# Optimization experiments

Hardware: AMD Instinct MI355X
Metric: run time of the kernel (lower is better)

Reference implementation:

```python
import jax, jax.numpy as jnp
import numpy as np

B, S, D, H = 2, 2048, 1024, 16
DH = D // H
EPS = 1e-5


def layer_norm(x, g, b):
    # OpenAI-style LN: epsilon inside the sqrt
    u = jnp.mean(x, axis=-1, keepdims=True)
    s = jnp.mean((x - u) ** 2, axis=-1, keepdims=True)
    return g * ((x - u) / jnp.sqrt(s + EPS)) + b


def setup_inputs() -> dict:
    key = jax.random.key(0)
    ks = jax.random.split(key, 8)
    std = 0.002  # Conv1D init std
    return {
        "x": jax.random.normal(ks[0], (B, S, D), dtype=jnp.float32),
        "mask": jnp.ones((B, S), dtype=jnp.bool_),
        "Wqkv": jax.random.normal(ks[1], (D, 3 * D), dtype=jnp.float32) * std,
        "bqkv": jnp.zeros((3 * D,), dtype=jnp.float32),
        "Wvw": jax.random.normal(ks[2], (D, D), dtype=jnp.float32) * std,
        "bvw": jnp.zeros((D,), dtype=jnp.float32),
        "g1": jnp.ones((D,), dtype=jnp.float32),
        "b1": jnp.zeros((D,), dtype=jnp.float32),
        "WA": jax.random.normal(ks[3], (D, 4 * D), dtype=jnp.float32) * std,
        "bA": jnp.zeros((4 * D,), dtype=jnp.float32),
        "WB": jax.random.normal(ks[4], (4 * D, D), dtype=jnp.float32) * std,
        "bB": jnp.zeros((D,), dtype=jnp.float32),
        "g2": jnp.ones((D,), dtype=jnp.float32),
        "b2": jnp.zeros((D,), dtype=jnp.float32),
    }


def reference(x, mask, Wqkv, bqkv, Wvw, bvw, g1, b1, WA, bA, WB, bB, g2, b2):
    maskf = mask.astype(x.dtype)                       # [B,S]
    x = x * maskf[:, :, None]
    # --- multi-head attention ---
    qkv = (x @ Wqkv + bqkv).reshape(B, S, 3, H, DH)    # [B,S,3,H,DH]
    q, k, v = qkv[:, :, 0], qkv[:, :, 1], qkv[:, :, 2]
    w = jnp.einsum('bshd,bzhd->bhsz', q, k) / jnp.sqrt(jnp.asarray(DH, x.dtype))
    causal = jnp.tril(jnp.ones((S, S), dtype=x.dtype)) # [S,S]
    wholemask = maskf[:, None, None, :] * causal[None, None]  # [B,1,S,S]
    w = w + jnp.log(wholemask)                         # additive log-mask (-inf where masked)
    w = jax.nn.softmax(w, axis=-1)
    vw = jnp.einsum('bhsz,bzhd->bshd', w, v).reshape(B, S, D)
    a = vw @ Wvw + bvw
    # --- residual + LN + MLP + LN ---
    n = layer_norm(x + a, g1, b1)
    m = jax.nn.relu(n @ WA + bA) @ WB + bB
    h = layer_norm(n + m, g2, b2)
    return h
```

## Files before the change

### kernel.cpp

```cpp
#include <hip/hip_runtime.h>
#include <stdint.h>

typedef unsigned short u16;
typedef __attribute__((ext_vector_type(8))) short short8;
typedef __attribute__((ext_vector_type(4))) float f32x4;

#define NB 2
#define NS 2048
#define ND 1024
#define NH 16
#define NDH 64
#define NBS (NB*NS)

__device__ __forceinline__ float bf2f(u16 u) {
  union { uint32_t i; float f; } c; c.i = ((uint32_t)u) << 16; return c.f;
}
__device__ __forceinline__ u16 f2bf(float f) {
  union { float f; uint32_t i; } c; c.f = f;
  uint32_t r = (c.i + 0x7fffu + ((c.i >> 16) & 1u)) >> 16;
  return (u16)r;
}

__global__ __launch_bounds__(256)
void k_f32_to_bf16(const float* __restrict__ X, u16* __restrict__ Y, int n4) {
  int i = blockIdx.x * 256 + threadIdx.x;
  if (i >= n4) return;
  float4 v = ((const float4*)X)[i];
  uint2 o;
  o.x = (uint32_t)f2bf(v.x) | ((uint32_t)f2bf(v.y) << 16);
  o.y = (uint32_t)f2bf(v.z) | ((uint32_t)f2bf(v.w) << 16);
  ((uint2*)Y)[i] = o;
}

__global__ __launch_bounds__(256)
void k_transpose_all(const float* __restrict__ Wqkv, const float* __restrict__ Wvw,
                     const float* __restrict__ WA, const float* __restrict__ WB,
                     u16* __restrict__ WqkvT, u16* __restrict__ WvwT,
                     u16* __restrict__ WAT, u16* __restrict__ WBT) {
  __shared__ float tile[32][33];
  int id = blockIdx.x;
  const float* W; u16* WT; int K, N, tid;
  if (id < 3072)      { W = Wqkv; WT = WqkvT; K = 1024; N = 3072; tid = id; }
  else if (id < 4096) { W = Wvw;  WT = WvwT;  K = 1024; N = 1024; tid = id - 3072; }
  else if (id < 8192) { W = WA;   WT = WAT;   K = 1024; N = 4096; tid = id - 4096; }
  else                { W = WB;   WT = WBT;   K = 4096; N = 1024; tid = id - 8192; }
  const int ntx = N >> 5;
  const int n0 = (tid % ntx) << 5, k0 = (tid / ntx) << 5;
  const int tx = threadIdx.x & 31, ty = threadIdx.x >> 5;
  #pragma unroll
  for (int j = 0; j < 4; ++j)
    tile[ty + 8*j][tx] = W[(size_t)(k0 + ty + 8*j) * N + (n0 + tx)];
  __syncthreads();
  #pragma unroll
  for (int j = 0; j < 4; ++j)
    WT[(size_t)(n0 + ty + 8*j) * K + (k0 + tx)] = f2bf(tile[tx][ty + 8*j]);
}

__global__ __launch_bounds__(256)
void k_vt(const u16* __restrict__ qkv, u16* __restrict__ Vt) {
  __shared__ u16 tile[64][72];
  const int zb = blockIdx.x;
  const int bh = blockIdx.y;
  const int b = bh >> 4, h = bh & 15;
  const int t = threadIdx.x;
  const int r = t >> 2, seg = (t & 3) * 16;
  const u16* src = qkv + ((size_t)(b * NS + zb * 64 + r)) * 3072 + 2048 + h * 64 + seg;
  *(short8*)(&tile[r][seg])     = *(const short8*)(src);
  *(short8*)(&tile[r][seg + 8]) = *(const short8*)(src + 8);
  __syncthreads();
  const int dh = t >> 2, zs = (t & 3) * 16;
  short8 o0, o1;
  #pragma unroll
  for (int i = 0; i < 8; ++i) o0[i] = (short)tile[zs + i][dh];
  #pragma unroll
  for (int i = 0; i < 8; ++i) o1[i] = (short)tile[zs + 8 + i][dh];
  u16* dst = Vt + (size_t)(bh * 64 + dh) * NS + zb * 64 + zs;
  *(short8*)(dst)     = o0;
  *(short8*)(dst + 8) = o1;
}

__device__ __forceinline__ void gload_lds16(const void* g, void* l) {
  __builtin_amdgcn_global_load_lds(
      (const __attribute__((address_space(1))) void*)(void*)(uintptr_t)g,
      (__attribute__((address_space(3))) void*)l, 16, 0, 0);
}

template<bool OUT_BF16, bool RELU>
__global__ __launch_bounds__(256)
void k_gemm_bt(const u16* __restrict__ A, const u16* __restrict__ BT,
               const float* __restrict__ bias, void* __restrict__ C,
               int M, int N, int Kstride, int Klen, size_t zCstride)
{
  __shared__ u16 As[128 * 64];
  __shared__ u16 Bs[128 * 64];
  const int t = threadIdx.x, wave = t >> 6, lane = t & 63;
  const int m0 = blockIdx.y * 128, n0 = blockIdx.x * 128;
  const int wr = wave >> 1, wc = wave & 1;
  const int koff = blockIdx.z * Klen;
  A  += koff;
  BT += koff;

  f32x4 acc[4][4] = {};

  int srow[4], scol[4];
  #pragma unroll
  for (int p = 0; p < 4; ++p) {
    int o = p * 4096 + wave * 1024 + lane * 16;
    int r = o >> 7;
    int cb = o & 127;
    srow[p] = r;
    scol[p] = (cb ^ ((r & 7) << 4)) >> 1;
  }

  const int nkt = Klen >> 6;
  for (int kt = 0; kt < nkt; ++kt) {
    const int k0 = kt << 6;
    #pragma unroll
    for (int p = 0; p < 4; ++p) {
      const u16* srcA = A  + (size_t)(m0 + srow[p]) * Kstride + k0 + scol[p];
      const u16* srcB = BT + (size_t)(n0 + srow[p]) * Kstride + k0 + scol[p];
      gload_lds16(srcA, (char*)As + p * 4096 + wave * 1024);
      gload_lds16(srcB, (char*)Bs + p * 4096 + wave * 1024);
    }
    asm volatile("s_waitcnt vmcnt(0)" ::: "memory");
    __syncthreads();

    #pragma unroll
    for (int kk = 0; kk < 2; ++kk) {
      const int cbase = kk * 64 + ((lane >> 4) << 4);
      short8 af[4], bf[4];
      #pragma unroll
      for (int mi = 0; mi < 4; ++mi) {
        int r = wr * 64 + mi * 16 + (lane & 15);
        af[mi] = *(const short8*)((const char*)As + r * 128 + (cbase ^ ((r & 7) << 4)));
      }
      #pragma unroll
      for (int nj = 0; nj < 4; ++nj) {
        int r = wc * 64 + nj * 16 + (lane & 15);
        bf[nj] = *(const short8*)((const char*)Bs + r * 128 + (cbase ^ ((r & 7) << 4)));
      }
      #pragma unroll
      for (int mi = 0; mi < 4; ++mi)
        #pragma unroll
        for (int nj = 0; nj < 4; ++nj)
          acc[mi][nj] = __builtin_amdgcn_mfma_f32_16x16x32_bf16(af[mi], bf[nj], acc[mi][nj], 0, 0, 0);
    }
    __syncthreads();
  }

  const int lr = (lane >> 4) << 2;
  const int lc = lane & 15;
  #pragma unroll
  for (int nj = 0; nj < 4; ++nj) {
    const int col = n0 + wc * 64 + nj * 16 + lc;
    const float bs = bias ? bias[col] : 0.f;
    #pragma unroll
    for (int mi = 0; mi < 4; ++mi) {
      const int row = m0 + wr * 64 + mi * 16 + lr;
      #pragma unroll
      for (int i = 0; i < 4; ++i) {
        float v = acc[mi][nj][i] + bs;
        if (RELU) v = fmaxf(v, 0.f);
        if (OUT_BF16) ((u16*)C)[blockIdx.z * zCstride + (size_t)(row + i) * N + col] = f2bf(v);
        else          ((float*)C)[blockIdx.z * zCstride + (size_t)(row + i) * N + col] = v;
      }
    }
  }
}

__device__ __forceinline__ void stage_tile256(const u16* __restrict__ src0, int K,
                                              char* ldsbase, int wave, int t) {
  const int rr = t >> 3;
  const int col = ((t & 7) ^ (rr & 7)) * 8;
  const u16* s = src0 + (size_t)rr * K + col;
  char* d = ldsbase + wave * 1024;
  #pragma unroll
  for (int j = 0; j < 4; ++j)
    gload_lds16(s + (size_t)(j * 64) * K, d + j * 8192);
}

__device__ __forceinline__ short8 lds_frag(const char* base, int row, int kkbyte) {
  return *(const short8*)(base + row * 128 + (kkbyte ^ ((row & 7) << 4)));
}

template<bool OUT_BF16, bool RELU>
__global__ __launch_bounds__(512, 2)
void k_gemm256(const u16* __restrict__ A, const u16* __restrict__ BT,
               const float* __restrict__ bias, void* __restrict__ C,
               int M, int N, int K, int nbx)
{
  extern __shared__ char lds[];
  const int t = threadIdx.x, wave = t >> 6, lane = t & 63;
  const int lg = lane >> 4, lq = lane & 15;
  const int wr = wave >> 2, wc = wave & 3;

  const int nwg = gridDim.x;
  const int sw = (blockIdx.x & 7) * (nwg >> 3) + (blockIdx.x >> 3);
  const int bx = sw % nbx, by = sw / nbx;
  const int m0 = by * 256, n0 = bx * 256;

  f32x4 acc[8][4] = {};
  short8 af[4][2], bf[4][2];

  const u16* Abase = A + (size_t)m0 * K;
  const u16* Bbase = BT + (size_t)n0 * K;

  stage_tile256(Abase, K, lds, wave, t);
  stage_tile256(Bbase, K, lds + 65536, wave, t);
  asm volatile("s_waitcnt vmcnt(0)" ::: "memory");
  __syncthreads();

  const int nkt = K >> 6;
  #pragma unroll 1
  for (int kt = 0; kt < nkt; ++kt) {
    const int cur = kt & 1;
    const char* pA = lds + cur * 32768;
    const char* pB = lds + 65536 + cur * 32768;
    char* qA = lds + (cur ^ 1) * 32768;
    char* qB = lds + 65536 + (cur ^ 1) * 32768;

    if (kt + 1 < nkt) {
      const int knext = (kt + 1) << 6;
      stage_tile256(Abase + knext, K, qA, wave, t);
      stage_tile256(Bbase + knext, K, qB, wave, t);
    }

    #pragma unroll
    for (int m = 0; m < 4; ++m) {
      const int row = wr * 128 + m * 16 + lq;
      af[m][0] = lds_frag(pA, row, lg * 16);
      af[m][1] = lds_frag(pA, row, 64 + lg * 16);
    }
    #pragma unroll
    for (int n = 0; n < 2; ++n) {
      const int row = wc * 64 + n * 16 + lq;
      bf[n][0] = lds_frag(pB, row, lg * 16);
      bf[n][1] = lds_frag(pB, row, 64 + lg * 16);
    }
    #pragma unroll
    for (int m = 0; m < 4; ++m)
      #pragma unroll
      for (int n = 0; n < 2; ++n) {
        acc[m][n] = __builtin_amdgcn_mfma_f32_16x16x32_bf16(af[m][0], bf[n][0], acc[m][n], 0, 0, 0);
        acc[m][n] = __builtin_amdgcn_mfma_f32_16x16x32_bf16(af[m][1], bf[n][1], acc[m][n], 0, 0, 0);
      }

    #pragma unroll
    for (int n = 2; n < 4; ++n) {
      const int row = wc * 64 + n * 16 + lq;
      bf[n][0] = lds_frag(pB, row, lg * 16);
      bf[n][1] = lds_frag(pB, row, 64 + lg * 16);
    }
    #pragma unroll
    for (int m = 0; m < 4; ++m)
      #pragma unroll
      for (int n = 2; n < 4; ++n) {
        acc[m][n] = __builtin_amdgcn_mfma_f32_16x16x32_bf16(af[m][0], bf[n][0], acc[m][n], 0, 0, 0);
        acc[m][n] = __builtin_amdgcn_mfma_f32_16x16x32_bf16(af[m][1], bf[n][1], acc[m][n], 0, 0, 0);
      }

    #pragma unroll
    for (int m = 0; m < 4; ++m) {
      const int row = wr * 128 + (m + 4) * 16 + lq;
      af[m][0] = lds_frag(pA, row, lg * 16);
      af[m][1] = lds_frag(pA, row, 64 + lg * 16);
    }
    #pragma unroll
    for (int m = 0; m < 4; ++m)
      #pragma unroll
      for (int n = 0; n < 2; ++n) {
        acc[m + 4][n] = __builtin_amdgcn_mfma_f32_16x16x32_bf16(af[m][0], bf[n][0], acc[m + 4][n], 0, 0, 0);
        acc[m + 4][n] = __builtin_amdgcn_mfma_f32_16x16x32_bf16(af[m][1], bf[n][1], acc[m + 4][n], 0, 0, 0);
      }

    #pragma unroll
    for (int m = 0; m < 4; ++m)
      #pragma unroll
      for (int n = 2; n < 4; ++n) {
        acc[m + 4][n] = __builtin_amdgcn_mfma_f32_16x16x32_bf16(af[m][0], bf[n][0], acc[m + 4][n], 0, 0, 0);
        acc[m + 4][n] = __builtin_amdgcn_mfma_f32_16x16x32_bf16(af[m][1], bf[n][1], acc[m + 4][n], 0, 0, 0);
      }

    asm volatile("s_waitcnt vmcnt(0)" ::: "memory");
    __syncthreads();
  }

  #pragma unroll
  for (int n = 0; n < 4; ++n) {
    const int col = n0 + wc * 64 + n * 16 + lq;
    const float bs = bias[col];
    #pragma unroll
    for (int m = 0; m < 8; ++m) {
      const int row = m0 + wr * 128 + m * 16 + lg * 4;
      #pragma unroll
      for (int i = 0; i < 4; ++i) {
        float v = acc[m][n][i] + bs;
        if (RELU) v = fmaxf(v, 0.f);
        if (OUT_BF16) ((u16*)C)[(size_t)(row + i) * N + col] = f2bf(v);
        else          ((float*)C)[(size_t)(row + i) * N + col] = v;
      }
    }
  }
}

__global__ __launch_bounds__(512)
void k_flash_attn(const u16* __restrict__ qkv, const u16* __restrict__ Vt,
                  u16* __restrict__ vw)
{
  __shared__ u16 Ks[2][64 * 64];
  __shared__ u16 Vts[2][64 * 64];
  __shared__ u16 P_lds[8][16 * 72];

  const int qb = 15 - (int)blockIdx.x;
  const int bh = blockIdx.y;
  const int b = bh >> 4, h = bh & 15;
  const int t = threadIdx.x, wave = t >> 6, lane = t & 63;
  const int lg = lane >> 4, lq = lane & 15;

  const int q0w = qb * 128 + wave * 16;

  const float QSC = 0.18033688f;
  short8 bq[2];
  {
    const u16* qrow = qkv + ((size_t)(b * NS + q0w + lq)) * 3072 + h * 64 + lg * 8;
    short8 r0 = *(const short8*)(qrow);
    short8 r1 = *(const short8*)(qrow + 32);
    union { short8 s; uint32_t u[4]; } o0, o1;
    #pragma unroll
    for (int p = 0; p < 4; ++p) {
      float a0 = bf2f((u16)r0[2*p]) * QSC, a1 = bf2f((u16)r0[2*p+1]) * QSC;
      float c0 = bf2f((u16)r1[2*p]) * QSC, c1 = bf2f((u16)r1[2*p+1]) * QSC;
      asm("v_cvt_pk_bf16_f32 %0, %1, %2" : "=v"(o0.u[p]) : "v"(a0), "v"(a1));
      asm("v_cvt_pk_bf16_f32 %0, %1, %2" : "=v"(o1.u[p]) : "v"(c0), "v"(c1));
    }
    bq[0] = o0.s; bq[1] = o1.s;
  }

  f32x4 o_acc[4] = {};
  float m_run = -1e30f, l_run = 0.f;

  const u16* kbase = qkv + (size_t)b * NS * 3072 + 1024 + h * 64;
  const u16* vtb   = Vt + (size_t)bh * 64 * NS;

  const int so = t * 16;
  const int sr = so >> 7;
  const int scb = (so & 127) ^ ((sr & 7) << 4);
  const int npairs = qb + 1;

  for (int kp = 0; kp < npairs; ++kp) {
    const int z0 = kp * 128;
    gload_lds16(kbase + (size_t)(z0 + sr) * 3072 + (scb >> 1),      (char*)Ks[0] + wave * 1024);
    gload_lds16(kbase + (size_t)(z0 + 64 + sr) * 3072 + (scb >> 1), (char*)Ks[1] + wave * 1024);
    gload_lds16(vtb + (size_t)sr * NS + z0 + (scb >> 1),            (char*)Vts[0] + wave * 1024);
    gload_lds16(vtb + (size_t)sr * NS + z0 + 64 + (scb >> 1),       (char*)Vts[1] + wave * 1024);
    asm volatile("s_waitcnt vmcnt(0)" ::: "memory");
    __syncthreads();

    #pragma unroll
    for (int sub = 0; sub < 2; ++sub) {
      const int zz = z0 + (sub << 6);
      if (zz <= q0w + 15) {
        f32x4 s_acc[4];
        __builtin_amdgcn_s_setprio(1);
        #pragma unroll
        for (int kb = 0; kb < 4; ++kb) {
          const int r = kb * 16 + lq;
          const int sw = (r & 7) << 4;
          short8 ak0 = *(const short8*)((const char*)Ks[sub] + r * 128 + ((lg * 16) ^ sw));
          short8 ak1 = *(const short8*)((const char*)Ks[sub] + r * 128 + ((64 + lg * 16) ^ sw));
          f32x4 zr = {0.f, 0.f, 0.f, 0.f};
          zr = __builtin_amdgcn_mfma_f32_16x16x32_bf16(ak0, bq[0], zr, 0, 0, 0);
          s_acc[kb] = __builtin_amdgcn_mfma_f32_16x16x32_bf16(ak1, bq[1], zr, 0, 0, 0);
        }
        __builtin_amdgcn_s_setprio(0);

        float sv[16];
        #pragma unroll
        for (int kb = 0; kb < 4; ++kb)
          #pragma unroll
          for (int i = 0; i < 4; ++i)
            sv[kb * 4 + i] = s_acc[kb][i];

        if (zz + 63 > q0w) {
          #pragma unroll
          for (int kb = 0; kb < 4; ++kb)
            #pragma unroll
            for (int i = 0; i < 4; ++i)
              if (zz + kb * 16 + lg * 4 + i > q0w + lq) sv[kb * 4 + i] = -1e30f;
        }

        float tm = -1e30f;
        #pragma unroll
        for (int j = 0; j < 16; ++j) tm = fmaxf(tm, sv[j]);
        tm = fmaxf(tm, __shfl_xor(tm, 16));
        tm = fmaxf(tm, __shfl_xor(tm, 32));

        if (!__all(tm <= m_run + 11.5415603f)) {
          const float m_new = fmaxf(m_run, tm);
          const float scl = __builtin_amdgcn_exp2f(m_run - m_new);
          float s0 = __shfl(scl, lg * 4 + 0);
          float s1 = __shfl(scl, lg * 4 + 1);
          float s2 = __shfl(scl, lg * 4 + 2);
          float s3 = __shfl(scl, lg * 4 + 3);
          #pragma unroll
          for (int nb = 0; nb < 4; ++nb) {
            o_acc[nb][0] *= s0; o_acc[nb][1] *= s1;
            o_acc[nb][2] *= s2; o_acc[nb][3] *= s3;
          }
          l_run *= scl;
          m_run = m_new;
        }

        float ts = 0.f;
        #pragma unroll
        for (int j = 0; j < 16; ++j) {
          float p = __builtin_amdgcn_exp2f(sv[j] - m_run);
          sv[j] = p; ts += p;
        }
        ts += __shfl_xor(ts, 16);
        ts += __shfl_xor(ts, 32);
        l_run += ts;

        #pragma unroll
        for (int kb = 0; kb < 4; ++kb) {
          uint32_t w0, w1;
          asm("v_cvt_pk_bf16_f32 %0, %1, %2" : "=v"(w0) : "v"(sv[kb*4+0]), "v"(sv[kb*4+1]));
          asm("v_cvt_pk_bf16_f32 %0, %1, %2" : "=v"(w1) : "v"(sv[kb*4+2]), "v"(sv[kb*4+3]));
          uint32_t* dst = (uint32_t*)&P_lds[wave][lq * 72 + kb * 16 + lg * 4];
          dst[0] = w0; dst[1] = w1;
        }
        short8 pa0 = *(const short8*)(&P_lds[wave][lq * 72 + lg * 8]);
        short8 pa1 = *(const short8*)(&P_lds[wave][lq * 72 + 32 + lg * 8]);

        __builtin_amdgcn_s_setprio(1);
        #pragma unroll
        for (int nb = 0; nb < 4; ++nb) {
          const int rv = nb * 16 + lq;
          const int swv = (rv & 7) << 4;
          short8 vb0 = *(const short8*)((const char*)Vts[sub] + rv * 128 + ((lg * 16) ^ swv));
          short8 vb1 = *(const short8*)((const char*)Vts[sub] + rv * 128 + ((64 + lg * 16) ^ swv));
          o_acc[nb] = __builtin_amdgcn_mfma_f32_16x16x32_bf16(pa0, vb0, o_acc[nb], 0, 0, 0);
          o_acc[nb] = __builtin_amdgcn_mfma_f32_16x16x32_bf16(pa1, vb1, o_acc[nb], 0, 0, 0);
        }
        __builtin_amdgcn_s_setprio(0);
      }
    }
    __syncthreads();
  }

  #pragma unroll
  for (int i = 0; i < 4; ++i) {
    const float rl = 1.0f / __shfl(l_run, lg * 4 + i);
    const int row = q0w + lg * 4 + i;
    #pragma unroll
    for (int nb = 0; nb < 4; ++nb) {
      const int col = h * 64 + nb * 16 + lq;
      vw[((size_t)b * NS + row) * ND + col] = f2bf(o_acc[nb][i] * rl);
    }
  }
}

template<bool WRITE_BF16>
__global__ __launch_bounds__(256)
void k_add_ln(const float* __restrict__ U, const float* __restrict__ V,
              const float* __restrict__ g, const float* __restrict__ beta,
              float* __restrict__ outf, u16* __restrict__ outb)
{
  const int row = blockIdx.x;
  const int t = threadIdx.x;
  const size_t base = (size_t)row * ND;
  float4 u = ((const float4*)(U + base))[t];
  float4 v = ((const float4*)(V + base))[t];
  float x0 = u.x + v.x, x1 = u.y + v.y, x2 = u.z + v.z, x3 = u.w + v.w;
  float s1 = x0 + x1 + x2 + x3;
  float s2 = x0*x0 + x1*x1 + x2*x2 + x3*x3;
  #pragma unroll
  for (int m = 32; m; m >>= 1) { s1 += __shfl_xor(s1, m); s2 += __shfl_xor(s2, m); }
  __shared__ float rs1[4], rs2[4];
  const int wave = t >> 6;
  if ((t & 63) == 0) { rs1[wave] = s1; rs2[wave] = s2; }
  __syncthreads();
  s1 = rs1[0] + rs1[1] + rs1[2] + rs1[3];
  s2 = rs2[0] + rs2[1] + rs2[2] + rs2[3];
  const float mean = s1 * (1.f / ND);
  const float var  = s2 * (1.f / ND) - mean * mean;
  const float rstd = rsqrtf(var + 1e-5f);
  float4 gg = ((const float4*)g)[t];
  float4 bb = ((const float4*)beta)[t];
  float y0 = gg.x * (x0 - mean) * rstd + bb.x;
  float y1 = gg.y * (x1 - mean) * rstd + bb.y;
  float y2 = gg.z * (x2 - mean) * rstd + bb.z;
  float y3 = gg.w * (x3 - mean) * rstd + bb.w;
  ((float4*)(outf + base))[t] = make_float4(y0, y1, y2, y3);
  if (WRITE_BF16) {
    uint2 ob;
    ob.x = (uint32_t)f2bf(y0) | ((uint32_t)f2bf(y1) << 16);
    ob.y = (uint32_t)f2bf(y2) | ((uint32_t)f2bf(y3) << 16);
    ((uint2*)(outb + base))[t] = ob;
  }
}

__global__ __launch_bounds__(256)
void k_add_ln2(const float* __restrict__ U, const float* __restrict__ P0,
               const float* __restrict__ P1, const float* __restrict__ bias,
               const float* __restrict__ g, const float* __restrict__ beta,
               float* __restrict__ outf)
{
  const int row = blockIdx.x;
  const int t = threadIdx.x;
  const size_t base = (size_t)row * ND;
  float4 u  = ((const float4*)(U + base))[t];
  float4 p0 = ((const float4*)(P0 + base))[t];
  float4 p1 = ((const float4*)(P1 + base))[t];
  float4 bv = ((const float4*)bias)[t];
  float x0 = u.x + p0.x + p1.x + bv.x;
  float x1 = u.y + p0.y + p1.y + bv.y;
  float x2 = u.z + p0.z + p1.z + bv.z;
  float x3 = u.w + p0.w + p1.w + bv.w;
  float s1 = x0 + x1 + x2 + x3;
  float s2 = x0*x0 + x1*x1 + x2*x2 + x3*x3;
  #pragma unroll
  for (int m = 32; m; m >>= 1) { s1 += __shfl_xor(s1, m); s2 += __shfl_xor(s2, m); }
  __shared__ float rs1[4], rs2[4];
  const int wave = t >> 6;
  if ((t & 63) == 0) { rs1[wave] = s1; rs2[wave] = s2; }
  __syncthreads();
  s1 = rs1[0] + rs1[1] + rs1[2] + rs1[3];
  s2 = rs2[0] + rs2[1] + rs2[2] + rs2[3];
  const float mean = s1 * (1.f / ND);
  const float var  = s2 * (1.f / ND) - mean * mean;
  const float rstd = rsqrtf(var + 1e-5f);
  float4 gg = ((const float4*)g)[t];
  float4 bb = ((const float4*)beta)[t];
  float y0 = gg.x * (x0 - mean) * rstd + bb.x;
  float y1 = gg.y * (x1 - mean) * rstd + bb.y;
  float y2 = gg.z * (x2 - mean) * rstd + bb.z;
  float y3 = gg.w * (x3 - mean) * rstd + bb.w;
  ((float4*)(outf + base))[t] = make_float4(y0, y1, y2, y3);
}

extern "C" void kernel_launch(void* const* d_in, const int* in_sizes, int n_in,
                              void* d_out, int out_size, void* d_ws, size_t ws_size,
                              hipStream_t stream) {
  const float* x    = (const float*)d_in[0];
  const float* Wqkv = (const float*)d_in[2];
  const float* bqkv = (const float*)d_in[3];
  const float* Wvw  = (const float*)d_in[4];
  const float* bvw  = (const float*)d_in[5];
  const float* g1   = (const float*)d_in[6];
  const float* b1   = (const float*)d_in[7];
  const float* WA   = (const float*)d_in[8];
  const float* bA   = (const float*)d_in[9];
  const float* WB   = (const float*)d_in[10];
  const float* bB   = (const float*)d_in[11];
  const float* g2   = (const float*)d_in[12];
  const float* b2   = (const float*)d_in[13];
  float* out = (float*)d_out;

  if (ws_size < 100663296) return;
  char* ws = (char*)d_ws;
  u16*  WqkvT = (u16*)(ws + 0);
  u16*  WvwT  = (u16*)(ws + 6291456);
  u16*  WAT   = (u16*)(ws + 8388608);
  u16*  WBT   = (u16*)(ws + 16777216);
  u16*  xb    = (u16*)(ws + 25165824);
  u16*  qkvb  = (u16*)(ws + 33554432);
  u16*  vwb   = (u16*)(ws + 58720256);
  float* a    = (float*)(ws + 67108864);
  float* nf   = (float*)(ws + 83886080);
  u16*  nb    = (u16*)(ws + 25165824);
  u16*  z     = (u16*)(ws + 33554432);
  u16*  Vtb   = (u16*)(ws + 67108864);
  float* pp   = (float*)ws;

  hipError_t e2 = hipFuncSetAttribute((const void*)&k_gemm256<true, true>,
                                      hipFuncAttributeMaxDynamicSharedMemorySize, 131072);
  const bool use256 = (e2 == hipSuccess);

  k_f32_to_bf16<<<dim3(NBS * ND / 4 / 256), 256, 0, stream>>>(x, xb, NBS * ND / 4);
  k_transpose_all<<<dim3(12288), 256, 0, stream>>>(Wqkv, Wvw, WA, WB, WqkvT, WvwT, WAT, WBT);

  k_gemm_bt<true, false><<<dim3(3 * ND / 128, NBS / 128, 1), 256, 0, stream>>>(
      xb, WqkvT, bqkv, qkvb, NBS, 3 * ND, ND, ND, 0);

  k_vt<<<dim3(NS / 64, NB * NH), 256, 0, stream>>>(qkvb, Vtb);
  k_flash_attn<<<dim3(NS / 128, NB * NH), 512, 0, stream>>>(qkvb, Vtb, vwb);

  k_gemm_bt<false, false><<<dim3(ND / 128, NBS / 128, 1), 256, 0, stream>>>(
      vwb, WvwT, bvw, a, NBS, ND, ND, ND, 0);

  k_add_ln<true><<<dim3(NBS), 256, 0, stream>>>(x, a, g1, b1, nf, nb);

  if (use256)
    k_gemm256<true, true><<<dim3((4 * ND / 256) * (NBS / 256)), 512, 131072, stream>>>(
        nb, WAT, bA, z, NBS, 4 * ND, ND, 4 * ND / 256);
  else
    k_gemm_bt<true, true><<<dim3(4 * ND / 128, NBS / 128, 1), 256, 0, stream>>>(
        nb, WAT, bA, z, NBS, 4 * ND, ND, ND, 0);

  k_gemm_bt<false, false><<<dim3(ND / 128, NBS / 128, 2), 256, 0, stream>>>(
      z, WBT, nullptr, pp, NBS, ND, 4 * ND, 2 * ND, (size_t)16777216);

  k_add_ln2<<<dim3(NBS), 256, 0, stream>>>(nf, pp, pp + 16777216, bB, g2, b2, out);
}
```

Before: 240.4 us.

## Pipeline 256-tile GEMM with fine-grained staging and route QKV and MLP-down through it

Restructures the 256x256 MFMA GEMM main loop so global-to-LDS loads are issued in quarter-tile chunks interleaved between MFMA groups, with raw s_barrier and s_setprio around compute, replacing the whole-tile double buffer with a waitcnt at the end of each step. The kernel gains split-K via blockIdx.z with per-split output offsets. The QKV projection and the MLP down-projection (split-K 4, bf16 partials) now use it, and a new LN kernel sums the four bf16 partials. This aims to hide load latency and raise occupancy of the large GEMMs, at the cost of bf16 rounding on the split-K partials and more complex synchronisation.

```diff
diff --git a/kernel.cpp b/kernel.cpp
--- a/kernel.cpp
+++ b/kernel.cpp
@@ -168,18 +168,7 @@
   }
 }
 
-__device__ __forceinline__ void stage_tile256(const u16* __restrict__ src0, int K,
-                                              char* ldsbase, int wave, int t) {
-  const int rr = t >> 3;
-  const int col = ((t & 7) ^ (rr & 7)) * 8;
-  const u16* s = src0 + (size_t)rr * K + col;
-  char* d = ldsbase + wave * 1024;
-  #pragma unroll
-  for (int j = 0; j < 4; ++j)
-    gload_lds16(s + (size_t)(j * 64) * K, d + j * 8192);
-}
-
-__device__ __forceinline__ short8 lds_frag(const char* base, int row, int kkbyte) {
+__device__ __forceinline__ short8 lds_frag8(const char* base, int row, int kkbyte) {
   return *(const short8*)(base + row * 128 + (kkbyte ^ ((row & 7) << 4)));
 }
 
@@ -187,9 +176,12 @@
 __global__ __launch_bounds__(512, 2)
 void k_gemm256(const u16* __restrict__ A, const u16* __restrict__ BT,
                const float* __restrict__ bias, void* __restrict__ C,
-               int M, int N, int K, int nbx)
+               int M, int N, int Kstride, int Klen, int nbx,
+               size_t zs1, size_t zs2)
 {
   extern __shared__ char lds[];
+  char* ldsA = lds;
+  char* ldsB = lds + 65536;
   const int t = threadIdx.x, wave = t >> 6, lane = t & 63;
   const int lg = lane >> 4, lq = lane & 15;
   const int wr = wave >> 2, wc = wave & 3;
@@ -199,96 +191,97 @@
   const int bx = sw % nbx, by = sw / nbx;
   const int m0 = by * 256, n0 = bx * 256;
 
+  const int koff = blockIdx.z * Klen;
+  A  += koff;
+  BT += koff;
+
+  const int rr = t >> 3;
+  const int scol = ((t & 7) ^ ((t >> 3) & 7)) * 8;
+  const u16* Asrc = A  + (size_t)(m0 + rr) * Kstride + scol;
+  const u16* Bsrc = BT + (size_t)(n0 + rr) * Kstride + scol;
+
+  const int nkt = Klen >> 6;
+  const int nht = nkt << 2;
+
   f32x4 acc[8][4] = {};
   short8 af[4][2], bf[4][2];
 
-  const u16* Abase = A + (size_t)m0 * K;
-  const u16* Bbase = BT + (size_t)n0 * K;
-
-  stage_tile256(Abase, K, lds, wave, t);
-  stage_tile256(Bbase, K, lds + 65536, wave, t);
-  asm volatile("s_waitcnt vmcnt(0)" ::: "memory");
-  __syncthreads();
-
-  const int nkt = K >> 6;
-  #pragma unroll 1
-  for (int kt = 0; kt < nkt; ++kt) {
-    const int cur = kt & 1;
-    const char* pA = lds + cur * 32768;
-    const char* pB = lds + 65536 + cur * 32768;
-    char* qA = lds + (cur ^ 1) * 32768;
-    char* qB = lds + 65536 + (cur ^ 1) * 32768;
-
-    if (kt + 1 < nkt) {
-      const int knext = (kt + 1) << 6;
-      stage_tile256(Abase + knext, K, qA, wave, t);
-      stage_tile256(Bbase + knext, K, qB, wave, t);
-    }
-
+  auto STAGE = [&](int s) {
+    if (s < nht) {
+      const int tile = s >> 2, part = s & 3, half = part & 1, slot = tile & 1;
+      const u16* src = (part < 2 ? Bsrc : Asrc) + (size_t)(half * 128) * Kstride + tile * 64;
+      char* d = (part < 2 ? ldsB : ldsA) + slot * 32768 + half * 16384 + wave * 1024;
+      gload_lds16(src, d);
+      gload_lds16(src + (size_t)64 * Kstride, d + 8192);
+    }
+  };
+  auto RDA = [&](int slot, int mo) {
+    const char* base = ldsA + slot * 32768;
     #pragma unroll
     for (int m = 0; m < 4; ++m) {
-      const int row = wr * 128 + m * 16 + lq;
-      af[m][0] = lds_frag(pA, row, lg * 16);
-      af[m][1] = lds_frag(pA, row, 64 + lg * 16);
-    }
+      const int row = wr * 128 + (mo + m) * 16 + lq;
+      af[m][0] = lds_frag8(base, row, lg * 16);
+      af[m][1] = lds_frag8(base, row, 64 + lg * 16);
+    }
+  };
+  auto RDB = [&](int slot, int no) {
+    const char* base = ldsB + slot * 32768;
     #pragma unroll
     for (int n = 0; n < 2; ++n) {
-      const int row = wc * 64 + n * 16 + lq;
-      bf[n][0] = lds_frag(pB, row, lg * 16);
-      bf[n][1] = lds_frag(pB, row, 64 + lg * 16);
-    }
+      const int row = wc * 64 + (no + n) * 16 + lq;
+      bf[no + n][0] = lds_frag8(base, row, lg * 16);
+      bf[no + n][1] = lds_frag8(base, row, 64 + lg * 16);
+    }
+  };
+  auto MF = [&](int mo, int no) {
+    __builtin_amdgcn_s_setprio(1);
     #pragma unroll
     for (int m = 0; m < 4; ++m)
       #pragma unroll
       for (int n = 0; n < 2; ++n) {
-        acc[m][n] = __builtin_amdgcn_mfma_f32_16x16x32_bf16(af[m][0], bf[n][0], acc[m][n], 0, 0, 0);
-        acc[m][n] = __builtin_amdgcn_mfma_f32_16x16x32_bf16(af[m][1], bf[n][1], acc[m][n], 0, 0, 0);
+        acc[mo + m][no + n] = __builtin_amdgcn_mfma_f32_16x16x32_bf16(af[m][0], bf[no + n][0], acc[mo + m][no + n], 0, 0, 0);
+        acc[mo + m][no + n] = __builtin_amdgcn_mfma_f32_16x16x32_bf16(af[m][1], bf[no + n][1], acc[mo + m][no + n], 0, 0, 0);
       }
-
-    #pragma unroll
-    for (int n = 2; n < 4; ++n) {
-      const int row = wc * 64 + n * 16 + lq;
-      bf[n][0] = lds_frag(pB, row, lg * 16);
-      bf[n][1] = lds_frag(pB, row, 64 + lg * 16);
-    }
-    #pragma unroll
-    for (int m = 0; m < 4; ++m)
-      #pragma unroll
-      for (int n = 2; n < 4; ++n) {
-        acc[m][n] = __builtin_amdgcn_mfma_f32_16x16x32_bf16(af[m][0], bf[n][0], acc[m][n], 0, 0, 0);
-        acc[m][n] = __builtin_amdgcn_mfma_f32_16x16x32_bf16(af[m][1], bf[n][1], acc[m][n], 0, 0, 0);
-      }
-
-    #pragma unroll
-    for (int m = 0; m < 4; ++m) {
-      const int row = wr * 128 + (m + 4) * 16 + lq;
-      af[m][0] = lds_frag(pA, row, lg * 16);
-      af[m][1] = lds_frag(pA, row, 64 + lg * 16);
-    }
-    #pragma unroll
-    for (int m = 0; m < 4; ++m)
-      #pragma unroll
-      for (int n = 0; n < 2; ++n) {
-        acc[m + 4][n] = __builtin_amdgcn_mfma_f32_16x16x32_bf16(af[m][0], bf[n][0], acc[m + 4][n], 0, 0, 0);
-        acc[m + 4][n] = __builtin_amdgcn_mfma_f32_16x16x32_bf16(af[m][1], bf[n][1], acc[m + 4][n], 0, 0, 0);
-      }
-
-    #pragma unroll
-    for (int m = 0; m < 4; ++m)
-      #pragma unroll
-      for (int n = 2; n < 4; ++n) {
-        acc[m + 4][n] = __builtin_amdgcn_mfma_f32_16x16x32_bf16(af[m][0], bf[n][0], acc[m + 4][n], 0, 0, 0);
-        acc[m + 4][n] = __builtin_amdgcn_mfma_f32_16x16x32_bf16(af[m][1], bf[n][1], acc[m + 4][n], 0, 0, 0);
-      }
-
-    asm volatile("s_waitcnt vmcnt(0)" ::: "memory");
-    __syncthreads();
-  }
-
+    __builtin_amdgcn_s_setprio(0);
+  };
+  #define BAR() asm volatile("s_barrier" ::: "memory")
+
+  #pragma unroll
+  for (int s = 0; s < 6; ++s) STAGE(s);
+  asm volatile("s_waitcnt vmcnt(4)" ::: "memory");
+  __syncthreads();
+
+  const int niter = nkt >> 1;
+  #pragma unroll 1
+  for (int i = 0; i < niter; ++i) {
+    const int bs = 8 * i + 6;
+    RDA(0, 0); RDB(0, 0); STAGE(bs + 0);
+    BAR(); MF(0, 0); BAR();
+    RDB(0, 2); STAGE(bs + 1);
+    BAR(); MF(0, 2); BAR();
+    RDA(0, 4); STAGE(bs + 2);
+    BAR(); MF(4, 0); BAR();
+    STAGE(bs + 3);
+    if (i == niter - 1) { asm volatile("s_waitcnt vmcnt(0)" ::: "memory"); }
+    else                { asm volatile("s_waitcnt vmcnt(4)" ::: "memory"); }
+    BAR(); MF(4, 2); BAR();
+    RDA(1, 0); RDB(1, 0); STAGE(bs + 4);
+    BAR(); MF(0, 0); BAR();
+    RDB(1, 2); STAGE(bs + 5);
+    BAR(); MF(0, 2); BAR();
+    RDA(1, 4); STAGE(bs + 6);
+    BAR(); MF(4, 0); BAR();
+    STAGE(bs + 7);
+    asm volatile("s_waitcnt vmcnt(4)" ::: "memory");
+    BAR(); MF(4, 2); BAR();
+  }
+  #undef BAR
+
+  const size_t zoff = (size_t)(blockIdx.z & 1) * zs1 + (size_t)(blockIdx.z >> 1) * zs2;
   #pragma unroll
   for (int n = 0; n < 4; ++n) {
     const int col = n0 + wc * 64 + n * 16 + lq;
-    const float bs = bias[col];
+    const float bs = bias ? bias[col] : 0.f;
     #pragma unroll
     for (int m = 0; m < 8; ++m) {
       const int row = m0 + wr * 128 + m * 16 + lg * 4;
@@ -296,8 +289,8 @@
       for (int i = 0; i < 4; ++i) {
         float v = acc[m][n][i] + bs;
         if (RELU) v = fmaxf(v, 0.f);
-        if (OUT_BF16) ((u16*)C)[(size_t)(row + i) * N + col] = f2bf(v);
-        else          ((float*)C)[(size_t)(row + i) * N + col] = v;
+        if (OUT_BF16) ((u16*)C)[zoff + (size_t)(row + i) * N + col] = f2bf(v);
+        else          ((float*)C)[zoff + (size_t)(row + i) * N + col] = v;
       }
     }
   }
@@ -501,6 +494,49 @@
 }
 
 __global__ __launch_bounds__(256)
+void k_add_ln2b(const float* __restrict__ U,
+                const u16* __restrict__ p0, const u16* __restrict__ p1,
+                const u16* __restrict__ p2, const u16* __restrict__ p3,
+                const float* __restrict__ bias,
+                const float* __restrict__ g, const float* __restrict__ beta,
+                float* __restrict__ outf)
+{
+  const int row = blockIdx.x;
+  const int t = threadIdx.x;
+  const size_t base = (size_t)row * ND;
+  float4 u  = ((const float4*)(U + base))[t];
+  float4 bv = ((const float4*)bias)[t];
+  uint2 a0 = ((const uint2*)(p0 + base))[t];
+  uint2 a1 = ((const uint2*)(p1 + base))[t];
+  uint2 a2 = ((const uint2*)(p2 + base))[t];
+  uint2 a3 = ((const uint2*)(p3 + base))[t];
+  float x0 = u.x + bv.x + bf2f((u16)(a0.x)) + bf2f((u16)(a1.x)) + bf2f((u16)(a2.x)) + bf2f((u16)(a3.x));
+  float x1 = u.y + bv.y + bf2f((u16)(a0.x >> 16)) + bf2f((u16)(a1.x >> 16)) + bf2f((u16)(a2.x >> 16)) + bf2f((u16)(a3.x >> 16));
+  float x2 = u.z + bv.z + bf2f((u16)(a0.y)) + bf2f((u16)(a1.y)) + bf2f((u16)(a2.y)) + bf2f((u16)(a3.y));
+  float x3 = u.w + bv.w + bf2f((u16)(a0.y >> 16)) + bf2f((u16)(a1.y >> 16)) + bf2f((u16)(a2.y >> 16)) + bf2f((u16)(a3.y >> 16));
+  float s1 = x0 + x1 + x2 + x3;
+  float s2 = x0*x0 + x1*x1 + x2*x2 + x3*x3;
+  #pragma unroll
+  for (int m = 32; m; m >>= 1) { s1 += __shfl_xor(s1, m); s2 += __shfl_xor(s2, m); }
+  __shared__ float rs1[4], rs2[4];
+  const int wave = t >> 6;
+  if ((t & 63) == 0) { rs1[wave] = s1; rs2[wave] = s2; }
+  __syncthreads();
+  s1 = rs1[0] + rs1[1] + rs1[2] + rs1[3];
+  s2 = rs2[0] + rs2[1] + rs2[2] + rs2[3];
+  const float mean = s1 * (1.f / ND);
+  const float var  = s2 * (1.f / ND) - mean * mean;
+  const float rstd = rsqrtf(var + 1e-5f);
+  float4 gg = ((const float4*)g)[t];
+  float4 bb = ((const float4*)beta)[t];
+  float y0 = gg.x * (x0 - mean) * rstd + bb.x;
+  float y1 = gg.y * (x1 - mean) * rstd + bb.y;
+  float y2 = gg.z * (x2 - mean) * rstd + bb.z;
+  float y3 = gg.w * (x3 - mean) * rstd + bb.w;
+  ((float4*)(outf + base))[t] = make_float4(y0, y1, y2, y3);
+}
+
+__global__ __launch_bounds__(256)
 void k_add_ln2(const float* __restrict__ U, const float* __restrict__ P0,
                const float* __restrict__ P1, const float* __restrict__ bias,
                const float* __restrict__ g, const float* __restrict__ beta,
@@ -571,17 +607,25 @@
   u16*  nb    = (u16*)(ws + 25165824);
   u16*  z     = (u16*)(ws + 33554432);
   u16*  Vtb   = (u16*)(ws + 67108864);
+  u16*  pb01  = (u16*)(ws + 0);
+  u16*  pb23  = (u16*)(ws + 67108864);
   float* pp   = (float*)ws;
 
+  hipError_t e1 = hipFuncSetAttribute((const void*)&k_gemm256<true, false>,
+                                      hipFuncAttributeMaxDynamicSharedMemorySize, 131072);
   hipError_t e2 = hipFuncSetAttribute((const void*)&k_gemm256<true, true>,
                                       hipFuncAttributeMaxDynamicSharedMemorySize, 131072);
-  const bool use256 = (e2 == hipSuccess);
+  const bool use256 = (e1 == hipSuccess) && (e2 == hipSuccess);
 
   k_f32_to_bf16<<<dim3(NBS * ND / 4 / 256), 256, 0, stream>>>(x, xb, NBS * ND / 4);
   k_transpose_all<<<dim3(12288), 256, 0, stream>>>(Wqkv, Wvw, WA, WB, WqkvT, WvwT, WAT, WBT);
 
-  k_gemm_bt<true, false><<<dim3(3 * ND / 128, NBS / 128, 1), 256, 0, stream>>>(
-      xb, WqkvT, bqkv, qkvb, NBS, 3 * ND, ND, ND, 0);
+  if (use256)
+    k_gemm256<true, false><<<dim3(192), 512, 131072, stream>>>(
+        xb, WqkvT, bqkv, qkvb, NBS, 3 * ND, ND, ND, 12, 0, 0);
+  else
+    k_gemm_bt<true, false><<<dim3(3 * ND / 128, NBS / 128, 1), 256, 0, stream>>>(
+        xb, WqkvT, bqkv, qkvb, NBS, 3 * ND, ND, ND, 0);
 
   k_vt<<<dim3(NS / 64, NB * NH), 256, 0, stream>>>(qkvb, Vtb);
   k_flash_attn<<<dim3(NS / 128, NB * NH), 512, 0, stream>>>(qkvb, Vtb, vwb);
@@ -592,14 +636,21 @@
   k_add_ln<true><<<dim3(NBS), 256, 0, stream>>>(x, a, g1, b1, nf, nb);
 
   if (use256)
-    k_gemm256<true, true><<<dim3((4 * ND / 256) * (NBS / 256)), 512, 131072, stream>>>(
-        nb, WAT, bA, z, NBS, 4 * ND, ND, 4 * ND / 256);
+    k_gemm256<true, true><<<dim3(256), 512, 131072, stream>>>(
+        nb, WAT, bA, z, NBS, 4 * ND, ND, ND, 16, 0, 0);
   else
     k_gemm_bt<true, true><<<dim3(4 * ND / 128, NBS / 128, 1), 256, 0, stream>>>(
         nb, WAT, bA, z, NBS, 4 * ND, ND, ND, 0);
 
-  k_gemm_bt<false, false><<<dim3(ND / 128, NBS / 128, 2), 256, 0, stream>>>(
-      z, WBT, nullptr, pp, NBS, ND, 4 * ND, 2 * ND, (size_t)16777216);
-
-  k_add_ln2<<<dim3(NBS), 256, 0, stream>>>(nf, pp, pp + 16777216, bB, g2, b2, out);
-}
+  if (use256) {
+    k_gemm256<true, false><<<dim3(64, 1, 4), 512, 131072, stream>>>(
+        z, WBT, nullptr, pb01, NBS, ND, 4 * ND, ND, 4,
+        (size_t)4194304, (size_t)(pb23 - pb01));
+    k_add_ln2b<<<dim3(NBS), 256, 0, stream>>>(
+        nf, pb01, pb01 + 4194304, pb23, pb23 + 4194304, bB, g2, b2, out);
+  } else {
+    k_gemm_bt<false, false><<<dim3(ND / 128, NBS / 128, 2), 256, 0, stream>>>(
+        z, WBT, nullptr, pp, NBS, ND, 4 * ND, 2 * ND, (size_t)16777216);
+    k_add_ln2<<<dim3(NBS), 256, 0, stream>>>(nf, pp, pp + 16777216, bB, g2, b2, out);
+  }
+}
```

New measurement: 244.6 us. Within noise of the previous version (+1.8%).
